# Performance work log

Hardware: AMD Instinct MI355X
Metric: run time of the kernel (lower is better)

## Reference

```python
import jax, jax.numpy as jnp
import numpy as np

D_MODEL = 256
D_STATE = 64
R_MIN, R_MAX, MAX_PHASE = 0.0, 1.0, 6.28


def setup_inputs() -> dict:
    key = jax.random.key(0)
    ks = jax.random.split(key, 8)
    u1 = jax.random.uniform(ks[0], (D_STATE,), dtype=jnp.float32)
    u2 = jax.random.uniform(ks[1], (D_STATE,), dtype=jnp.float32)
    nu_log = jnp.log(-0.5 * jnp.log(u1 * (R_MAX**2 - R_MIN**2) + R_MIN**2))
    theta_log = jnp.log(u2 * MAX_PHASE)
    sB = 1.0 / np.sqrt(2 * D_STATE)
    sC = 1.0 / np.sqrt(D_STATE)
    B_re = jax.random.normal(ks[2], (D_MODEL, D_STATE), dtype=jnp.float32) * sB
    B_im = jax.random.normal(ks[3], (D_MODEL, D_STATE), dtype=jnp.float32) * sB
    C_re = jax.random.normal(ks[4], (D_MODEL, D_STATE), dtype=jnp.float32) * sC
    C_im = jax.random.normal(ks[5], (D_MODEL, D_STATE), dtype=jnp.float32) * sC
    D = jax.random.normal(ks[6], (D_MODEL,), dtype=jnp.float32)
    x = jax.random.normal(ks[7], (4, 8192, D_MODEL), dtype=jnp.float32)
    return {"x": x, "nu_log": nu_log, "theta_log": theta_log,
            "B_re": B_re, "B_im": B_im, "C_re": C_re, "C_im": C_im, "D": D}


def reference(x, nu_log, theta_log, B_re, B_im, C_re, C_im, D):
    B, L, H = x.shape
    # diagonal transition: Lambda = exp(-exp(nu) + i*exp(theta)); Lambda^k = exp(k*log_lambda)
    log_lambda = -jnp.exp(nu_log) + 1j * jnp.exp(theta_log)          # (n,)
    k = jnp.arange(L, dtype=jnp.float32)
    Lambda_k = jnp.exp(k[:, None] * log_lambda[None, :])              # (L, n) complex
    CB = (C_re + 1j * C_im) * (B_re + 1j * B_im)                      # (H, n)
    kernels = jnp.einsum('hn,ln->hl', CB, Lambda_k).real              # (H, L)
    # FFT (causal, linear) convolution per channel
    n_fft = 2 * L
    x_f = jnp.fft.rfft(x, n=n_fft, axis=1)                            # (B, L+1, H)
    k_f = jnp.fft.rfft(kernels, n=n_fft, axis=1)                      # (H, L+1)
    y_f = x_f * k_f.T[None]                                           # (B, L+1, H)
    y = jnp.fft.irfft(y_f, n=n_fft, axis=1)[:, :L, :]
    return y + x * D[None, None, :]
```

## Files before the change

kernel.cpp:

```cpp
#include <hip/hip_runtime.h>
#include <hip/hip_bf16.h>

#define BB   4
#define LL   8192
#define HH   256
#define NN   64
#define NSEG 128
#define LSEG 64
#define YCS  258

typedef __attribute__((ext_vector_type(8))) short  short8;
typedef __attribute__((ext_vector_type(4))) float  float4v;
typedef __attribute__((ext_vector_type(4))) int    int4v;


__device__ __forceinline__ float ldF(const void* p, size_t i, int isbf) {
    return isbf ? __bfloat162float(((const __hip_bfloat16*)p)[i])
                : ((const float*)p)[i];
}

__device__ __forceinline__ int sniff1(const void* p) {
    const unsigned int* d = (const unsigned int*)p;
    int nbf = 0, nrand = 0;
    #pragma unroll
    for (int i = 0; i < 32; ++i) {
        unsigned int lo = d[i] & 0xFFFFu;
        unsigned int e  = (lo >> 7) & 0xFFu;
        if (lo == 0u) {  }
        else if (e >= 90u && e <= 140u) nbf++;
        else nrand++;
    }
    return (nrand == 0 && nbf >= 8) ? 1 : 0;
}

__device__ __forceinline__ unsigned int packbf(float re, float im) {
    __hip_bfloat16 hr = __float2bfloat16(re);
    __hip_bfloat16 hi = __float2bfloat16(im);
    return ((unsigned int)*(unsigned short*)&hi << 16)
         |  (unsigned int)*(unsigned short*)&hr;
}
__device__ __forceinline__ float unpkre(unsigned int u) {
    unsigned short s = (unsigned short)(u & 0xFFFFu);
    return __bfloat162float(*(__hip_bfloat16*)&s);
}
__device__ __forceinline__ float unpkim(unsigned int u) {
    unsigned short s = (unsigned short)(u >> 16);
    return __bfloat162float(*(__hip_bfloat16*)&s);
}

__global__ __launch_bounds__(256) void k_setup(
    const void* x, const void* nu_log, const void* theta_log,
    const void* B_re, const void* B_im,
    const void* C_re, const void* C_im,
    const void* D, int* flags,
    float* lam, float* lam64, float* Df, float* CBt,
    float* PsegRe, float* PsegIm)
{
    __shared__ int sf[8];
    {
        int tt = threadIdx.x;
        if (tt < 8) {
            const void* ps[8] = {x, nu_log, theta_log, B_re, B_im,
                                 C_re, C_im, D};
            sf[tt] = sniff1(ps[tt]);
        }
        __syncthreads();
        if (blockIdx.x == 0 && tt < 8) flags[tt] = sf[tt];
    }
    int t = blockIdx.x * 256 + threadIdx.x;
    if (t < NN) {
        float nu = expf(ldF(nu_log, t, sf[1]));
        float th = expf(ldF(theta_log, t, sf[2]));
        float a  = expf(-nu);
        lam[2*t]   = a * cosf(th);
        lam[2*t+1] = a * sinf(th);
        float a64 = expf(-64.0f * nu);
        float ph  = 64.0f * th;
        lam64[2*t]   = a64 * cosf(ph);
        lam64[2*t+1] = a64 * sinf(ph);
    }
    if (t < HH) Df[t] = ldF(D, t, sf[7]);
    if (t < HH * NN) {
        int h = t >> 6, n = t & 63;
        float bre = ldF(B_re, h*NN+n, sf[3]);
        float bim = ldF(B_im, h*NN+n, sf[4]);
        float cre = ldF(C_re, h*NN+n, sf[5]);
        float cim = ldF(C_im, h*NN+n, sf[6]);
        CBt[(n*2+0)*HH + h] = cre*bre - cim*bim;
        CBt[(n*2+1)*HH + h] = cre*bim + cim*bre;
    }
    if (t < 64 * 64) {
        int l = t >> 6, n = t & 63;
        float nu = expf(ldF(nu_log, n, sf[1]));
        float th = expf(ldF(theta_log, n, sf[2]));
        float fp = (float)(63 - l);
        float ar = expf(-fp * nu);
        PsegRe[t] = ar * cosf(fp * th);
        PsegIm[t] = ar * sinf(fp * th);
    }
}

__global__ __launch_bounds__(256) void k_ktab(
    const float* __restrict__ CBt, const float* __restrict__ PsegRe,
    const float* __restrict__ PsegIm, const float* __restrict__ lam64,
    float* __restrict__ Ktab,
    short* __restrict__ VreT, short* __restrict__ VimnT,
    short* __restrict__ PreH, short* __restrict__ PreL,
    short* __restrict__ PimH, short* __restrict__ PimL)
{
    int t = blockIdx.x * 256 + threadIdx.x;
    int h = t >> 6, j = t & 63;
    float acc = 0.f;
    for (int n = 0; n < NN; ++n)
        acc += CBt[(2*n)*HH + h]   * PsegRe[(63-j)*64 + n]
             - CBt[(2*n+1)*HH + h] * PsegIm[(63-j)*64 + n];
    Ktab[j*HH + h] = acc;
    if (t < 64*64) {
        int tau = t >> 6, n = t & 63;
        float vr, vi;
        if (tau < 63) {
            vr =  PsegRe[(62-tau)*64 + n];
            vi = -PsegIm[(62-tau)*64 + n];
        } else {
            vr =  lam64[2*n];
            vi = -lam64[2*n+1];
        }
        __hip_bfloat16 br = __float2bfloat16(vr);
        __hip_bfloat16 bi = __float2bfloat16(vi);
        VreT[tau*64 + n]  = *(short*)&br;
        VimnT[tau*64 + n] = *(short*)&bi;

        int n2 = t >> 6, l2 = t & 63;
        float pr = PsegRe[l2*64 + n2];
        float pi = PsegIm[l2*64 + n2];
        __hip_bfloat16 prh = __float2bfloat16(pr);
        __hip_bfloat16 prl = __float2bfloat16(pr - __bfloat162float(prh));
        __hip_bfloat16 pih = __float2bfloat16(pi);
        __hip_bfloat16 pil = __float2bfloat16(pi - __bfloat162float(pih));
        PreH[t] = *(short*)&prh;
        PreL[t] = *(short*)&prl;
        PimH[t] = *(short*)&pih;
        PimL[t] = *(short*)&pil;
    }
}

template<bool ISBF>
__device__ __forceinline__ void segsum_body(
    const void* __restrict__ x, size_t sb, unsigned int* __restrict__ xsh,
    const short* __restrict__ PreH, const short* __restrict__ PreL,
    const short* __restrict__ PimH, const short* __restrict__ PimL,
    unsigned int* __restrict__ Apack, size_t abase, int w, int q, int l15)
{
    int t = threadIdx.x;
    if (ISBF) {
        const short8* xp = (const short8*)((const short*)x + sb);
        #pragma unroll
        for (int i = 0; i < 8; ++i) {
            short8 v = xp[i*256 + t];
            int e = (i*256 + t) * 8;
            #pragma unroll
            for (int k = 0; k < 8; ++k)
                xsh[e + k] = (unsigned int)(unsigned short)v[k];
        }
    } else {
        const float4v* xp = (const float4v*)((const float*)x + sb);
        #pragma unroll
        for (int i = 0; i < 16; ++i) {
            float4v v = xp[i*256 + t];
            int e = (i*256 + t) * 4;
            #pragma unroll
            for (int k = 0; k < 4; ++k) {
                float xf = v[k];
                __hip_bfloat16 hv = __float2bfloat16(xf);
                __hip_bfloat16 lv = __float2bfloat16(xf - __bfloat162float(hv));
                xsh[e + k] = ((unsigned int)*(unsigned short*)&lv << 16)
                           |  (unsigned int)*(unsigned short*)&hv;
            }
        }
    }
    __syncthreads();

    #pragma unroll
    for (int nt = 0; nt < 4; ++nt) {
        short8 xh[2], xl[2];
        #pragma unroll
        for (int ks = 0; ks < 2; ++ks)
            #pragma unroll
            for (int j = 0; j < 8; ++j) {
                unsigned int u = xsh[(ks*32 + q*8 + j)*256 + w*64 + nt*16 + l15];
                xh[ks][j] = (short)(u & 0xFFFFu);
                if (!ISBF) xl[ks][j] = (short)(u >> 16);
            }
        #pragma unroll
        for (int mt = 0; mt < 4; ++mt) {
            float4v ar = {0.f, 0.f, 0.f, 0.f};
            float4v ai = {0.f, 0.f, 0.f, 0.f};
            #pragma unroll
            for (int ks = 0; ks < 2; ++ks) {
                int off = (mt*16 + l15)*64 + ks*32 + q*8;
                short8 prh = *(const short8*)(PreH + off);
                short8 pih = *(const short8*)(PimH + off);
                short8 prl = *(const short8*)(PreL + off);
                short8 pil = *(const short8*)(PimL + off);
                ar = __builtin_amdgcn_mfma_f32_16x16x32_bf16(prh, xh[ks], ar, 0, 0, 0);
                ai = __builtin_amdgcn_mfma_f32_16x16x32_bf16(pih, xh[ks], ai, 0, 0, 0);
                ar = __builtin_amdgcn_mfma_f32_16x16x32_bf16(prl, xh[ks], ar, 0, 0, 0);
                ai = __builtin_amdgcn_mfma_f32_16x16x32_bf16(pil, xh[ks], ai, 0, 0, 0);
                if (!ISBF) {
                    ar = __builtin_amdgcn_mfma_f32_16x16x32_bf16(prh, xl[ks], ar, 0, 0, 0);
                    ai = __builtin_amdgcn_mfma_f32_16x16x32_bf16(pih, xl[ks], ai, 0, 0, 0);
                }
            }
            #pragma unroll
            for (int r = 0; r < 4; ++r) {
                int n = mt*16 + q*4 + r;
                Apack[abase + (size_t)n*64 + nt*16 + l15] = packbf(ar[r], ai[r]);
            }
        }
    }
}

__global__ __launch_bounds__(256) void k_segsum(
    const void* __restrict__ x,
    const short* __restrict__ PreH, const short* __restrict__ PreL,
    const short* __restrict__ PimH, const short* __restrict__ PimL,
    const int* __restrict__ flags, unsigned int* __restrict__ Apack)
{
    __shared__ unsigned int xsh[64 * 256];
    int bk = blockIdx.x;
    int s  = bk & (NSEG - 1);
    int b  = bk >> 7;
    int w    = threadIdx.x >> 6;
    int lane = threadIdx.x & 63;
    int q = lane >> 4, l15 = lane & 15;

    size_t sb    = ((size_t)(b*LL) + s*64) * HH;
    size_t abase = (((size_t)(b*4 + w) * NSEG + s) * NN) * 64;

    if (flags[0]) segsum_body<true >(x, sb, xsh, PreH, PreL, PimH, PimL, Apack, abase, w, q, l15);
    else          segsum_body<false>(x, sb, xsh, PreH, PreL, PimH, PimL, Apack, abase, w, q, l15);
}

__global__ __launch_bounds__(256) void k_scan(
    const float* __restrict__ lam64, const float* __restrict__ CBt,
    unsigned int* __restrict__ Apack)
{
    int w    = blockIdx.x * 4 + (threadIdx.x >> 6);
    int lane = threadIdx.x & 63;
    int n    = w & 63;
    int hg   = (w >> 6) & 3;
    int b    = w >> 8;
    int h    = hg*64 + lane;

    float lre = lam64[2*n], lim = lam64[2*n+1];
    float cbre = CBt[(2*n)*HH + h], cbim = CBt[(2*n+1)*HH + h];
    float sre = 0.f, sim = 0.f;
    size_t base0 = (((size_t)(b*4 + hg) * NSEG) * NN + n) * 64 + lane;

    unsigned int curU[32], nxtU[32];
    #pragma unroll
    for (int k = 0; k < 32; ++k)
        curU[k] = Apack[base0 + (size_t)k * NN * 64];
    #pragma unroll
    for (int blk = 0; blk < 4; ++blk) {
        if (blk < 3) {
            #pragma unroll
            for (int k = 0; k < 32; ++k)
                nxtU[k] = Apack[base0 + (size_t)((blk+1)*32 + k) * NN * 64];
        }
        #pragma unroll
        for (int k = 0; k < 32; ++k) {
            size_t idx = base0 + (size_t)(blk*32 + k) * NN * 64;
            float are = unpkre(curU[k]);
            float aim = unpkim(curU[k]);
            float ure = cbre*sre - cbim*sim;
            float uim = cbre*sim + cbim*sre;
            Apack[idx] = packbf(ure, uim);
            float t2 = fmaf(lre, sre, fmaf(-lim, sim, are));
            sim = fmaf(lre, sim, fmaf(lim, sre, aim));
            sre = t2;
        }
        #pragma unroll
        for (int k = 0; k < 32; ++k) curU[k] = nxtU[k];
    }
}

template<bool ISBF, int U>
__device__ __forceinline__ void conv_u(
    const void* __restrict__ x, const float* __restrict__ Df,
    const float* __restrict__ Ktab, const float* __restrict__ yc,
    int b, int s, int h, float* __restrict__ y)
{
    int g0 = s*64 + U*16;
    size_t rbase = ((size_t)b*LL + g0)*HH + h;
    float xv[16], yv[16];
    float dh = Df[h];
    #pragma unroll
    for (int t = 0; t < 16; ++t) {
        float xl;
        if (ISBF) xl = __bfloat162float(((const __hip_bfloat16*)x)[rbase + (size_t)t*HH]);
        else      xl = ((const float*)x)[rbase + (size_t)t*HH];
        xv[t] = xl;
        yv[t] = fmaf(dh, xl, yc[(U*16 + t)*YCS + h]);
    }
    float kreg[16*U + 16];
    #pragma unroll
    for (int j = 0; j < 16*U + 16; ++j) kreg[j] = Ktab[j*HH + h];
    #pragma unroll
    for (int j = 0; j < 16; ++j)
        #pragma unroll
        for (int t = j; t < 16; ++t) yv[t] = fmaf(kreg[j], xv[t-j], yv[t]);
    #pragma unroll
    for (int m = 0; m < 16*U; ++m) {
        float xm;
        size_t ra = ((size_t)b*LL + (g0 - 1 - m))*HH + h;
        if (ISBF) xm = __bfloat162float(((const __hip_bfloat16*)x)[ra]);
        else      xm = ((const float*)x)[ra];
        #pragma unroll
        for (int t = 0; t < 16; ++t) yv[t] = fmaf(kreg[t+1+m], xm, yv[t]);
    }
    #pragma unroll
    for (int t = 0; t < 16; ++t) y[rbase + (size_t)t*HH] = yv[t];
}

template<bool ISBF>
__device__ __forceinline__ void cc_body(
    const short* __restrict__ VreT, const short* __restrict__ VimnT,
    const unsigned int* __restrict__ Upack, const void* __restrict__ x,
    const float* __restrict__ Df, const float* __restrict__ Ktab,
    float* yc, int b, int s, float* __restrict__ y)
{
    int t = threadIdx.x;

    int w = t >> 6, lane = t & 63;
    int hg = w & 3, nt = w >> 2;
    int q = lane >> 4, l15 = lane & 15;
    size_t ubase = (((size_t)(b*4 + hg) * NSEG + s) * NN) * 64;

    int l = nt*16 + l15;
    short8 bre[2], bim[2];
    #pragma unroll
    for (int ks = 0; ks < 2; ++ks)
        #pragma unroll
        for (int j = 0; j < 8; ++j) {
            int n = ks*32 + q*8 + j;
            unsigned int u = Upack[ubase + (size_t)n*64 + l];
            bre[ks][j] = (short)(u & 0xFFFFu);
            bim[ks][j] = (short)(u >> 16);
        }
    int h = hg*64 + l;
    #pragma unroll
    for (int mt = 0; mt < 4; ++mt) {
        float4v acc = {0.f, 0.f, 0.f, 0.f};
        #pragma unroll
        for (int ks = 0; ks < 2; ++ks) {
            int off = (mt*16 + l15)*64 + ks*32 + q*8;
            short8 afr = *(const short8*)(VreT + off);
            short8 afi = *(const short8*)(VimnT + off);
            acc = __builtin_amdgcn_mfma_f32_16x16x32_bf16(afr, bre[ks], acc, 0, 0, 0);
            acc = __builtin_amdgcn_mfma_f32_16x16x32_bf16(afi, bim[ks], acc, 0, 0, 0);
        }
        #pragma unroll
        for (int r = 0; r < 4; ++r) {
            int tau = mt*16 + q*4 + r;
            yc[tau*YCS + h] = acc[r];
        }
    }

    __syncthreads();

    int u = w >> 2;
    int h2 = hg*64 + lane;
    switch (u) {
        case 0: conv_u<ISBF,0>(x, Df, Ktab, yc, b, s, h2, y); break;
        case 1: conv_u<ISBF,1>(x, Df, Ktab, yc, b, s, h2, y); break;
        case 2: conv_u<ISBF,2>(x, Df, Ktab, yc, b, s, h2, y); break;
        case 3: conv_u<ISBF,3>(x, Df, Ktab, yc, b, s, h2, y); break;
    }
}

__global__ __launch_bounds__(1024) void k_cc(
    const short* __restrict__ VreT, const short* __restrict__ VimnT,
    const unsigned int* __restrict__ Upack, const void* __restrict__ x,
    const float* __restrict__ Df, const float* __restrict__ Ktab,
    const int* __restrict__ flags, float* __restrict__ y)
{
    __shared__ float yc[64 * YCS];
    int bk = blockIdx.x;
    int s  = bk & (NSEG - 1);
    int b  = bk >> 7;
    if (flags[0]) cc_body<true >(VreT, VimnT, Upack, x, Df, Ktab, yc, b, s, y);
    else          cc_body<false>(VreT, VimnT, Upack, x, Df, Ktab, yc, b, s, y);
}

extern "C" void kernel_launch(void* const* d_in, const int* in_sizes, int n_in,
                              void* d_out, int out_size, void* d_ws, size_t ws_size,
                              hipStream_t stream)
{
    const void* x  = d_in[0];
    const void* nu = d_in[1];
    const void* th = d_in[2];
    const void* Br = d_in[3];
    const void* Bi = d_in[4];
    const void* Cr = d_in[5];
    const void* Ci = d_in[6];
    const void* D  = d_in[7];

    char* ws = (char*)d_ws;
    float* lam    = (float*)(ws);
    float* lam64  = (float*)(ws + 512);
    int*   flags  = (int*)(ws + 1024);
    float* Df     = (float*)(ws + 1088);
    float* CBt    = (float*)(ws + 2112);
    float* Ktab   = (float*)(ws + 133184);
    short* VreT   = (short*)(ws + 198720);
    short* VimnT  = (short*)(ws + 206912);
    float* PsegRe = (float*)(ws + 215104);
    float* PsegIm = (float*)(ws + 231744);
    short* PreH   = (short*)(ws + 248128);
    short* PreL   = (short*)(ws + 256320);
    short* PimH   = (short*)(ws + 264512);
    short* PimL   = (short*)(ws + 272704);
    unsigned int* Apack = (unsigned int*)(ws + 294912);
    float* yout = (float*)d_out;

    k_setup<<<dim3(64), dim3(256), 0, stream>>>(x, nu, th, Br, Bi, Cr, Ci, D,
                                                flags, lam, lam64, Df, CBt,
                                                PsegRe, PsegIm);
    k_ktab<<<dim3(64), dim3(256), 0, stream>>>(CBt, PsegRe, PsegIm, lam64,
                                               Ktab, VreT, VimnT,
                                               PreH, PreL, PimH, PimL);
    k_segsum<<<dim3(512), dim3(256), 0, stream>>>(x, PreH, PreL, PimH, PimL,
                                                  flags, Apack);
    k_scan<<<dim3(256), dim3(256), 0, stream>>>(lam64, CBt, Apack);
    k_cc<<<dim3(512), dim3(1024), 0, stream>>>(VreT, VimnT, Apack,
                                               x, Df, Ktab, flags, yout);
}
```

Baseline: 176.4 us.

## Fuse setup and kernel-table launches, split segment-sum blocks by channel half

Merges the two small setup kernels into one launch by recomputing the decay powers and C·B products inline instead of staging them through workspace, which removes one launch and its dependency. Separately, the segment-sum kernel now gives each block only half of the 256 channels, doubling the grid to 1024 blocks and halving shared memory per block. This should improve occupancy and load balance for the MFMA segment sums. The cost is redundant transcendental and parameter work in the init kernel, plus strided x loads per row.

```diff
diff --git a/kernel.cpp b/kernel.cpp
--- a/kernel.cpp
+++ b/kernel.cpp
@@ -48,99 +48,93 @@
     return __bfloat162float(*(__hip_bfloat16*)&s);
 }
 
-__global__ __launch_bounds__(256) void k_setup(
+__global__ __launch_bounds__(256) void k_init(
     const void* x, const void* nu_log, const void* theta_log,
     const void* B_re, const void* B_im,
     const void* C_re, const void* C_im,
     const void* D, int* flags,
-    float* lam, float* lam64, float* Df, float* CBt,
-    float* PsegRe, float* PsegIm)
+    float* lam64, float* Df, float* CBt,
+    float* Ktab, short* VreT, short* VimnT,
+    short* PreH, short* PreL, short* PimH, short* PimL)
 {
     __shared__ int sf[8];
-    {
-        int tt = threadIdx.x;
-        if (tt < 8) {
-            const void* ps[8] = {x, nu_log, theta_log, B_re, B_im,
-                                 C_re, C_im, D};
-            sf[tt] = sniff1(ps[tt]);
-        }
-        __syncthreads();
-        if (blockIdx.x == 0 && tt < 8) flags[tt] = sf[tt];
-    }
-    int t = blockIdx.x * 256 + threadIdx.x;
-    if (t < NN) {
-        float nu = expf(ldF(nu_log, t, sf[1]));
-        float th = expf(ldF(theta_log, t, sf[2]));
-        float a  = expf(-nu);
-        lam[2*t]   = a * cosf(th);
-        lam[2*t+1] = a * sinf(th);
-        float a64 = expf(-64.0f * nu);
-        float ph  = 64.0f * th;
-        lam64[2*t]   = a64 * cosf(ph);
-        lam64[2*t+1] = a64 * sinf(ph);
-    }
-    if (t < HH) Df[t] = ldF(D, t, sf[7]);
-    if (t < HH * NN) {
-        int h = t >> 6, n = t & 63;
-        float bre = ldF(B_re, h*NN+n, sf[3]);
-        float bim = ldF(B_im, h*NN+n, sf[4]);
-        float cre = ldF(C_re, h*NN+n, sf[5]);
-        float cim = ldF(C_im, h*NN+n, sf[6]);
-        CBt[(n*2+0)*HH + h] = cre*bre - cim*bim;
-        CBt[(n*2+1)*HH + h] = cre*bim + cim*bre;
-    }
-    if (t < 64 * 64) {
-        int l = t >> 6, n = t & 63;
-        float nu = expf(ldF(nu_log, n, sf[1]));
-        float th = expf(ldF(theta_log, n, sf[2]));
-        float fp = (float)(63 - l);
-        float ar = expf(-fp * nu);
-        PsegRe[t] = ar * cosf(fp * th);
-        PsegIm[t] = ar * sinf(fp * th);
-    }
-}
-
-__global__ __launch_bounds__(256) void k_ktab(
-    const float* __restrict__ CBt, const float* __restrict__ PsegRe,
-    const float* __restrict__ PsegIm, const float* __restrict__ lam64,
-    float* __restrict__ Ktab,
-    short* __restrict__ VreT, short* __restrict__ VimnT,
-    short* __restrict__ PreH, short* __restrict__ PreL,
-    short* __restrict__ PimH, short* __restrict__ PimL)
-{
-    int t = blockIdx.x * 256 + threadIdx.x;
-    int h = t >> 6, j = t & 63;
-    float acc = 0.f;
-    for (int n = 0; n < NN; ++n)
-        acc += CBt[(2*n)*HH + h]   * PsegRe[(63-j)*64 + n]
-             - CBt[(2*n+1)*HH + h] * PsegIm[(63-j)*64 + n];
-    Ktab[j*HH + h] = acc;
-    if (t < 64*64) {
-        int tau = t >> 6, n = t & 63;
-        float vr, vi;
-        if (tau < 63) {
-            vr =  PsegRe[(62-tau)*64 + n];
-            vi = -PsegIm[(62-tau)*64 + n];
-        } else {
-            vr =  lam64[2*n];
-            vi = -lam64[2*n+1];
-        }
-        __hip_bfloat16 br = __float2bfloat16(vr);
-        __hip_bfloat16 bi = __float2bfloat16(vi);
-        VreT[tau*64 + n]  = *(short*)&br;
-        VimnT[tau*64 + n] = *(short*)&bi;
-
-        int n2 = t >> 6, l2 = t & 63;
-        float pr = PsegRe[l2*64 + n2];
-        float pi = PsegIm[l2*64 + n2];
-        __hip_bfloat16 prh = __float2bfloat16(pr);
-        __hip_bfloat16 prl = __float2bfloat16(pr - __bfloat162float(prh));
-        __hip_bfloat16 pih = __float2bfloat16(pi);
-        __hip_bfloat16 pil = __float2bfloat16(pi - __bfloat162float(pih));
-        PreH[t] = *(short*)&prh;
-        PreL[t] = *(short*)&prl;
-        PimH[t] = *(short*)&pih;
-        PimL[t] = *(short*)&pil;
+    int tid = threadIdx.x;
+    if (tid < 8) {
+        const void* ps[8] = {x, nu_log, theta_log, B_re, B_im, C_re, C_im, D};
+        sf[tid] = sniff1(ps[tid]);
+    }
+    __syncthreads();
+    if (blockIdx.x == 0 && tid < 8) flags[tid] = sf[tid];
+
+    if (blockIdx.x < 64) {
+        int t = blockIdx.x * 256 + tid;
+        if (t < NN) {
+            float nu = expf(ldF(nu_log, t, sf[1]));
+            float th = expf(ldF(theta_log, t, sf[2]));
+            float a64 = expf(-64.0f * nu);
+            float ph  = 64.0f * th;
+            lam64[2*t]   = a64 * cosf(ph);
+            lam64[2*t+1] = a64 * sinf(ph);
+        }
+        if (t < HH) Df[t] = ldF(D, t, sf[7]);
+        if (t < HH * NN) {
+            int h = t >> 6, n = t & 63;
+            float bre = ldF(B_re, h*NN+n, sf[3]);
+            float bim = ldF(B_im, h*NN+n, sf[4]);
+            float cre = ldF(C_re, h*NN+n, sf[5]);
+            float cim = ldF(C_im, h*NN+n, sf[6]);
+            CBt[(n*2+0)*HH + h] = cre*bre - cim*bim;
+            CBt[(n*2+1)*HH + h] = cre*bim + cim*bre;
+        }
+    } else {
+        int t = (blockIdx.x - 64) * 256 + tid;
+        int h = t >> 6, j = t & 63;
+        float fj = (float)j;
+        float acc = 0.f;
+        for (int n = 0; n < NN; ++n) {
+            float nu = expf(ldF(nu_log, n, sf[1]));
+            float th = expf(ldF(theta_log, n, sf[2]));
+            float ar = expf(-fj * nu);
+            float prn = ar * cosf(fj * th);
+            float pin = ar * sinf(fj * th);
+            float bre = ldF(B_re, h*NN+n, sf[3]);
+            float bim = ldF(B_im, h*NN+n, sf[4]);
+            float cre = ldF(C_re, h*NN+n, sf[5]);
+            float cim = ldF(C_im, h*NN+n, sf[6]);
+            float cbre = cre*bre - cim*bim;
+            float cbim = cre*bim + cim*bre;
+            acc += cbre * prn - cbim * pin;
+        }
+        Ktab[j*HH + h] = acc;
+        if (t < 64*64) {
+            int tau = t >> 6, n = t & 63;
+            float nu = expf(ldF(nu_log, n, sf[1]));
+            float th = expf(ldF(theta_log, n, sf[2]));
+            float fp = (float)(tau + 1);
+            float ar = expf(-fp * nu);
+            float vr =  ar * cosf(fp * th);
+            float vi = -(ar * sinf(fp * th));
+            __hip_bfloat16 br = __float2bfloat16(vr);
+            __hip_bfloat16 bi = __float2bfloat16(vi);
+            VreT[tau*64 + n]  = *(short*)&br;
+            VimnT[tau*64 + n] = *(short*)&bi;
+
+            int n2 = t >> 6, l2 = t & 63;
+            float nu2 = expf(ldF(nu_log, n2, sf[1]));
+            float th2 = expf(ldF(theta_log, n2, sf[2]));
+            float fp2 = (float)(63 - l2);
+            float ar2 = expf(-fp2 * nu2);
+            float pr = ar2 * cosf(fp2 * th2);
+            float pi = ar2 * sinf(fp2 * th2);
+            __hip_bfloat16 prh = __float2bfloat16(pr);
+            __hip_bfloat16 prl = __float2bfloat16(pr - __bfloat162float(prh));
+            __hip_bfloat16 pih = __float2bfloat16(pi);
+            __hip_bfloat16 pil = __float2bfloat16(pi - __bfloat162float(pih));
+            PreH[t] = *(short*)&prh;
+            PreL[t] = *(short*)&prl;
+            PimH[t] = *(short*)&pih;
+            PimL[t] = *(short*)&pil;
+        }
     }
 }
 
@@ -149,30 +143,35 @@
     const void* __restrict__ x, size_t sb, unsigned int* __restrict__ xsh,
     const short* __restrict__ PreH, const short* __restrict__ PreL,
     const short* __restrict__ PimH, const short* __restrict__ PimL,
-    unsigned int* __restrict__ Apack, size_t abase, int w, int q, int l15)
+    unsigned int* __restrict__ Apack, size_t abase0,
+    int half, int w, int q, int l15)
 {
     int t = threadIdx.x;
     if (ISBF) {
-        const short8* xp = (const short8*)((const short*)x + sb);
-        #pragma unroll
-        for (int i = 0; i < 8; ++i) {
-            short8 v = xp[i*256 + t];
-            int e = (i*256 + t) * 8;
+        const short* xb = (const short*)x + sb + half*128;
+        #pragma unroll
+        for (int i = 0; i < 4; ++i) {
+            int idx = i*256 + t;
+            int r = idx >> 4, oc = idx & 15;
+            short8 v = *(const short8*)(xb + (size_t)r*HH + oc*8);
+            int e = r*128 + oc*8;
             #pragma unroll
             for (int k = 0; k < 8; ++k)
                 xsh[e + k] = (unsigned int)(unsigned short)v[k];
         }
     } else {
-        const float4v* xp = (const float4v*)((const float*)x + sb);
-        #pragma unroll
-        for (int i = 0; i < 16; ++i) {
-            float4v v = xp[i*256 + t];
-            int e = (i*256 + t) * 4;
+        const float* xf = (const float*)x + sb + half*128;
+        #pragma unroll
+        for (int i = 0; i < 8; ++i) {
+            int idx = i*256 + t;
+            int r = idx >> 5, qc = idx & 31;
+            float4v v = *(const float4v*)(xf + (size_t)r*HH + qc*4);
+            int e = r*128 + qc*4;
             #pragma unroll
             for (int k = 0; k < 4; ++k) {
-                float xf = v[k];
-                __hip_bfloat16 hv = __float2bfloat16(xf);
-                __hip_bfloat16 lv = __float2bfloat16(xf - __bfloat162float(hv));
+                float xv2 = v[k];
+                __hip_bfloat16 hv = __float2bfloat16(xv2);
+                __hip_bfloat16 lv = __float2bfloat16(xv2 - __bfloat162float(hv));
                 xsh[e + k] = ((unsigned int)*(unsigned short*)&lv << 16)
                            |  (unsigned int)*(unsigned short*)&hv;
             }
@@ -181,13 +180,19 @@
     __syncthreads();
 
     #pragma unroll
-    for (int nt = 0; nt < 4; ++nt) {
+    for (int nt = 0; nt < 2; ++nt) {
+        int colLoc = w*32 + nt*16 + l15;
+        int colAbs = half*128 + colLoc;
+        int hgG    = colAbs >> 6;
+        int colIn  = colAbs & 63;
+        size_t abase = abase0 + (size_t)hgG * ((size_t)NSEG * NN * 64);
+
         short8 xh[2], xl[2];
         #pragma unroll
         for (int ks = 0; ks < 2; ++ks)
             #pragma unroll
             for (int j = 0; j < 8; ++j) {
-                unsigned int u = xsh[(ks*32 + q*8 + j)*256 + w*64 + nt*16 + l15];
+                unsigned int u = xsh[(ks*32 + q*8 + j)*128 + colLoc];
                 xh[ks][j] = (short)(u & 0xFFFFu);
                 if (!ISBF) xl[ks][j] = (short)(u >> 16);
             }
@@ -214,7 +219,7 @@
             #pragma unroll
             for (int r = 0; r < 4; ++r) {
                 int n = mt*16 + q*4 + r;
-                Apack[abase + (size_t)n*64 + nt*16 + l15] = packbf(ar[r], ai[r]);
+                Apack[abase + (size_t)n*64 + colIn] = packbf(ar[r], ai[r]);
             }
         }
     }
@@ -226,19 +231,20 @@
     const short* __restrict__ PimH, const short* __restrict__ PimL,
     const int* __restrict__ flags, unsigned int* __restrict__ Apack)
 {
-    __shared__ unsigned int xsh[64 * 256];
+    __shared__ unsigned int xsh[64 * 128];
     int bk = blockIdx.x;
-    int s  = bk & (NSEG - 1);
-    int b  = bk >> 7;
+    int half = bk & 1;
+    int s  = (bk >> 1) & (NSEG - 1);
+    int b  = bk >> 8;
     int w    = threadIdx.x >> 6;
     int lane = threadIdx.x & 63;
     int q = lane >> 4, l15 = lane & 15;
 
-    size_t sb    = ((size_t)(b*LL) + s*64) * HH;
-    size_t abase = (((size_t)(b*4 + w) * NSEG + s) * NN) * 64;
-
-    if (flags[0]) segsum_body<true >(x, sb, xsh, PreH, PreL, PimH, PimL, Apack, abase, w, q, l15);
-    else          segsum_body<false>(x, sb, xsh, PreH, PreL, PimH, PimL, Apack, abase, w, q, l15);
+    size_t sb     = ((size_t)(b*LL) + s*64) * HH;
+    size_t abase0 = (((size_t)(b*4) * NSEG + s) * NN) * 64;
+
+    if (flags[0]) segsum_body<true >(x, sb, xsh, PreH, PreL, PimH, PimL, Apack, abase0, half, w, q, l15);
+    else          segsum_body<false>(x, sb, xsh, PreH, PreL, PimH, PimL, Apack, abase0, half, w, q, l15);
 }
 
 __global__ __launch_bounds__(256) void k_scan(
@@ -407,7 +413,6 @@
     const void* D  = d_in[7];
 
     char* ws = (char*)d_ws;
-    float* lam    = (float*)(ws);
     float* lam64  = (float*)(ws + 512);
     int*   flags  = (int*)(ws + 1024);
     float* Df     = (float*)(ws + 1088);
@@ -415,8 +420,6 @@
     float* Ktab   = (float*)(ws + 133184);
     short* VreT   = (short*)(ws + 198720);
     short* VimnT  = (short*)(ws + 206912);
-    float* PsegRe = (float*)(ws + 215104);
-    float* PsegIm = (float*)(ws + 231744);
     short* PreH   = (short*)(ws + 248128);
     short* PreL   = (short*)(ws + 256320);
     short* PimH   = (short*)(ws + 264512);
@@ -424,14 +427,12 @@
     unsigned int* Apack = (unsigned int*)(ws + 294912);
     float* yout = (float*)d_out;
 
-    k_setup<<<dim3(64), dim3(256), 0, stream>>>(x, nu, th, Br, Bi, Cr, Ci, D,
-                                                flags, lam, lam64, Df, CBt,
-                                                PsegRe, PsegIm);
-    k_ktab<<<dim3(64), dim3(256), 0, stream>>>(CBt, PsegRe, PsegIm, lam64,
-                                               Ktab, VreT, VimnT,
-                                               PreH, PreL, PimH, PimL);
-    k_segsum<<<dim3(512), dim3(256), 0, stream>>>(x, PreH, PreL, PimH, PimL,
-                                                  flags, Apack);
+    k_init<<<dim3(128), dim3(256), 0, stream>>>(x, nu, th, Br, Bi, Cr, Ci, D,
+                                                flags, lam64, Df, CBt,
+                                                Ktab, VreT, VimnT,
+                                                PreH, PreL, PimH, PimL);
+    k_segsum<<<dim3(1024), dim3(256), 0, stream>>>(x, PreH, PreL, PimH, PimL,
+                                                   flags, Apack);
     k_scan<<<dim3(256), dim3(256), 0, stream>>>(lam64, CBt, Apack);
     k_cc<<<dim3(512), dim3(1024), 0, stream>>>(VreT, VimnT, Apack,
                                                x, Df, Ktab, flags, yout);
```

Result: slower. 194.5 us (+10.2%).
